# Kernel optimization log

Hardware: AMD Instinct MI355X
Metric: run time of the kernel (lower is better)

## Reference

```python
import jax, jax.numpy as jnp
import jax.lax as lax
import numpy as np
import math

B, T_FRAMES, H, W = 32, 8, 14, 14
C, CA = 768, 384
L = H * W + 1


def setup_inputs() -> dict:
    key = jax.random.key(0)
    ks = jax.random.split(key, 7)
    s = 0.02
    return {
        "x": jax.random.normal(ks[0], (B * T_FRAMES, L, C), dtype=jnp.float32),
        "W1": jax.random.normal(ks[1], (CA, C), dtype=jnp.float32) * s,
        "b1": jnp.zeros((CA,), dtype=jnp.float32),
        "conv_w": jax.random.normal(ks[2], (CA, 1, 3, 3, 3), dtype=jnp.float32) * s,
        "conv_b": jnp.zeros((CA,), dtype=jnp.float32),
        "W2": jax.random.normal(ks[3], (C, CA), dtype=jnp.float32) * s,
        "b2": jnp.zeros((C,), dtype=jnp.float32),
        "T": T_FRAMES,
    }


def reference(x, W1, b1, conv_w, conv_b, W2, b2, T):
    BT, Lx, Cx = x.shape
    Bb = BT // T
    Ca = W1.shape[0]
    Hh = Ww = int(round(math.sqrt(Lx - 1)))
    # fc1 on all tokens except CLS: [BT, L-1, Ca]
    h = jnp.einsum("blc,ac->bla", x[:, 1:, :], W1) + b1
    # -> [B, Ca, T, H, W] for depthwise 3d conv (groups = Ca)
    h = h.reshape(Bb, T, Hh, Ww, Ca).transpose(0, 4, 1, 2, 3)
    h = lax.conv_general_dilated(
        h, conv_w,
        window_strides=(1, 1, 1),
        padding=[(1, 1), (1, 1), (1, 1)],
        dimension_numbers=("NCDHW", "OIDHW", "NCDHW"),
        feature_group_count=Ca,
    ) + conv_b[None, :, None, None, None]
    # back to [BT, L-1, Ca]
    h = h.transpose(0, 2, 3, 4, 1).reshape(BT, Lx - 1, Ca)
    # fc2: [BT, L-1, C]
    h = jnp.einsum("bla,ca->blc", h, W2) + b2
    # residual add onto non-CLS tokens
    return x.at[:, 1:, :].add(h)
```

## Files before the change

### kernel.cpp

```cpp
#include <hip/hip_runtime.h>
#include <stdint.h>

#define BTOT   256
#define LX     197
#define CDIM   768
#define CADIM  384
#define TFR    8
#define HHH    14
#define WWW    14
#define LM1    196
#define MTOT   50176

typedef unsigned short u16;
typedef short          bf16x8 __attribute__((ext_vector_type(8)));
typedef unsigned short u16x4  __attribute__((ext_vector_type(4)));
typedef unsigned short u16x8  __attribute__((ext_vector_type(8)));
typedef float          f32x4  __attribute__((ext_vector_type(4)));

static __device__ __forceinline__ u16 f2bf(float f) {
  union { float f; uint32_t u; } v; v.f = f;
  uint32_t u = v.u;
  return (u16)((u + 0x7FFFu + ((u >> 16) & 1u)) >> 16);
}
static __device__ __forceinline__ float bf2f(u16 h) {
  union { uint32_t u; float f; } v; v.u = ((uint32_t)h) << 16;
  return v.f;
}

__global__ void prep_x(const float4* __restrict__ x, u16x4* __restrict__ xb, int nvec) {
  int stride = gridDim.x * blockDim.x;
  for (int i = blockIdx.x * blockDim.x + threadIdx.x; i < nvec; i += stride) {
    float4 v = x[i];
    u16x4 o;
    o[0] = f2bf(v.x); o[1] = f2bf(v.y); o[2] = f2bf(v.z); o[3] = f2bf(v.w);
    xb[i] = o;
  }
}

__global__ void prep_w(const float* __restrict__ W1, const float* __restrict__ W2,
                       const float* __restrict__ cw, u16* __restrict__ w1b,
                       u16* __restrict__ w2b, float* __restrict__ cwT) {
  int i = blockIdx.x * blockDim.x + threadIdx.x;
  if (i < CADIM * CDIM) { w1b[i] = f2bf(W1[i]); w2b[i] = f2bf(W2[i]); }
  if (i < CADIM * 27) {
    int a = i / 27; int tap = i - a * 27;
    cwT[tap * CADIM + a] = cw[i];
  }
}

__global__ void cls_copy(const float4* __restrict__ x, float4* __restrict__ out) {
  int i = blockIdx.x * blockDim.x + threadIdx.x;
  int bt = i / 192;
  int c  = i - bt * 192;
  int idx = bt * (LX * CDIM / 4) + c;
  out[idx] = x[idx];
}

#define BK  64
#define LDK 72

__global__ __launch_bounds__(256) void fc1_gemm(
    const u16* __restrict__ A,
    const u16* __restrict__ Bw,
    const float* __restrict__ bias,
    u16* __restrict__ Hout)
{
  __shared__ __align__(16) u16 As[128 * LDK];
  __shared__ __align__(16) u16 Bs[128 * LDK];
  const int tid = threadIdx.x;
  const int m0 = blockIdx.x * 128;
  const int n0 = blockIdx.y * 128;
  const int lane = tid & 63;
  const int wv = tid >> 6;
  const int wm = (wv & 1) * 64;
  const int wn = (wv >> 1) * 64;
  const int lm = lane & 15;
  const int lk = lane >> 4;

  f32x4 acc[4][4];
#pragma unroll
  for (int i = 0; i < 4; i++)
#pragma unroll
    for (int j = 0; j < 4; j++) acc[i][j] = (f32x4)0.0f;

  int arow_off[4], brow_off[4];
#pragma unroll
  for (int it = 0; it < 4; ++it) {
    int chunk = it * 256 + tid;
    int row = chunk >> 3;
    int tok = m0 + row;
    int bt = tok / LM1;
    int l = tok - bt * LM1;
    arow_off[it] = (bt * LX + 1 + l) * CDIM;
    brow_off[it] = (n0 + row) * CDIM;
  }

  for (int k0 = 0; k0 < CDIM; k0 += BK) {
#pragma unroll
    for (int it = 0; it < 4; ++it) {
      int chunk = it * 256 + tid;
      int row = chunk >> 3;
      int cc = chunk & 7;
      *(bf16x8*)&As[row * LDK + cc * 8] = *(const bf16x8*)(A + arow_off[it] + k0 + cc * 8);
      *(bf16x8*)&Bs[row * LDK + cc * 8] = *(const bf16x8*)(Bw + brow_off[it] + k0 + cc * 8);
    }
    __syncthreads();
#pragma unroll
    for (int kk = 0; kk < BK; kk += 32) {
      bf16x8 af[4], bfr[4];
#pragma unroll
      for (int i = 0; i < 4; i++)
        af[i] = *(const bf16x8*)&As[(wm + i * 16 + lm) * LDK + kk + lk * 8];
#pragma unroll
      for (int j = 0; j < 4; j++)
        bfr[j] = *(const bf16x8*)&Bs[(wn + j * 16 + lm) * LDK + kk + lk * 8];
#pragma unroll
      for (int i = 0; i < 4; i++)
#pragma unroll
        for (int j = 0; j < 4; j++)
          acc[i][j] = __builtin_amdgcn_mfma_f32_16x16x32_bf16(af[i], bfr[j], acc[i][j], 0, 0, 0);
    }
    __syncthreads();
  }

#pragma unroll
  for (int i = 0; i < 4; i++) {
    int rbase = m0 + wm + i * 16 + lk * 4;
#pragma unroll
    for (int j = 0; j < 4; j++) {
      int col = n0 + wn + j * 16 + lm;
      float bv = bias[col];
#pragma unroll
      for (int r = 0; r < 4; r++)
        Hout[(rbase + r) * CADIM + col] = f2bf(acc[i][j][r] + bv);
    }
  }
}

__global__ __launch_bounds__(256) void dwconv(
    const u16* __restrict__ h1, const float* __restrict__ cwT,
    const float* __restrict__ cb, u16* __restrict__ h2)
{
  int idx = blockIdx.x * blockDim.x + threadIdx.x;
  int tok = idx / 48;
  int cg = idx - tok * 48;
  int a0 = cg * 8;
  int bt = tok / LM1;
  int l = tok - bt * LM1;
  int t = bt & 7;
  int b = bt >> 3;
  int h = l / 14;
  int w = l - h * 14;

  float acc[8];
#pragma unroll
  for (int c = 0; c < 8; c++) acc[c] = cb[a0 + c];

#pragma unroll
  for (int dt = -1; dt <= 1; ++dt) {
    int tt = t + dt;
    if (tt < 0 || tt >= TFR) continue;
#pragma unroll
    for (int dh = -1; dh <= 1; ++dh) {
      int hh = h + dh;
      if (hh < 0 || hh >= HHH) continue;
#pragma unroll
      for (int dw = -1; dw <= 1; ++dw) {
        int ww = w + dw;
        if (ww < 0 || ww >= WWW) continue;
        int ntok = (b * TFR + tt) * LM1 + hh * 14 + ww;
        bf16x8 v = *(const bf16x8*)(h1 + ntok * CADIM + a0);
        int tap = (dt + 1) * 9 + (dh + 1) * 3 + (dw + 1);
        const float* wp = cwT + tap * CADIM + a0;
#pragma unroll
        for (int c = 0; c < 8; c++)
          acc[c] += bf2f((u16)v[c]) * wp[c];
      }
    }
  }
  u16x8 o;
#pragma unroll
  for (int c = 0; c < 8; c++) o[c] = f2bf(acc[c]);
  *(u16x8*)(h2 + tok * CADIM + a0) = o;
}

__global__ __launch_bounds__(256) void fc2_gemm(
    const u16* __restrict__ A,
    const u16* __restrict__ Bw,
    const float* __restrict__ bias,
    const float* __restrict__ x,
    float* __restrict__ out)
{
  __shared__ __align__(16) u16 As[128 * LDK];
  __shared__ __align__(16) u16 Bs[128 * LDK];
  const int tid = threadIdx.x;
  const int m0 = blockIdx.x * 128;
  const int n0 = blockIdx.y * 128;
  const int lane = tid & 63;
  const int wv = tid >> 6;
  const int wm = (wv & 1) * 64;
  const int wn = (wv >> 1) * 64;
  const int lm = lane & 15;
  const int lk = lane >> 4;

  f32x4 acc[4][4];
#pragma unroll
  for (int i = 0; i < 4; i++)
#pragma unroll
    for (int j = 0; j < 4; j++) acc[i][j] = (f32x4)0.0f;

  int arow_off[4], brow_off[4];
#pragma unroll
  for (int it = 0; it < 4; ++it) {
    int chunk = it * 256 + tid;
    int row = chunk >> 3;
    arow_off[it] = (m0 + row) * CADIM;
    brow_off[it] = (n0 + row) * CADIM;
  }

  for (int k0 = 0; k0 < CADIM; k0 += BK) {
#pragma unroll
    for (int it = 0; it < 4; ++it) {
      int chunk = it * 256 + tid;
      int row = chunk >> 3;
      int cc = chunk & 7;
      *(bf16x8*)&As[row * LDK + cc * 8] = *(const bf16x8*)(A + arow_off[it] + k0 + cc * 8);
      *(bf16x8*)&Bs[row * LDK + cc * 8] = *(const bf16x8*)(Bw + brow_off[it] + k0 + cc * 8);
    }
    __syncthreads();
#pragma unroll
    for (int kk = 0; kk < BK; kk += 32) {
      bf16x8 af[4], bfr[4];
#pragma unroll
      for (int i = 0; i < 4; i++)
        af[i] = *(const bf16x8*)&As[(wm + i * 16 + lm) * LDK + kk + lk * 8];
#pragma unroll
      for (int j = 0; j < 4; j++)
        bfr[j] = *(const bf16x8*)&Bs[(wn + j * 16 + lm) * LDK + kk + lk * 8];
#pragma unroll
      for (int i = 0; i < 4; i++)
#pragma unroll
        for (int j = 0; j < 4; j++)
          acc[i][j] = __builtin_amdgcn_mfma_f32_16x16x32_bf16(af[i], bfr[j], acc[i][j], 0, 0, 0);
    }
    __syncthreads();
  }

#pragma unroll
  for (int i = 0; i < 4; i++) {
    int rbase = m0 + wm + i * 16 + lk * 4;
#pragma unroll
    for (int r = 0; r < 4; r++) {
      int tok = rbase + r;
      int bt = tok / LM1;
      int l = tok - bt * LM1;
      int orow = (bt * LX + 1 + l) * CDIM;
#pragma unroll
      for (int j = 0; j < 4; j++) {
        int col = n0 + wn + j * 16 + lm;
        out[orow + col] = x[orow + col] + acc[i][j][r] + bias[col];
      }
    }
  }
}

extern "C" void kernel_launch(void* const* d_in, const int* in_sizes, int n_in,
                              void* d_out, int out_size, void* d_ws, size_t ws_size,
                              hipStream_t stream) {
  const float* x  = (const float*)d_in[0];
  const float* W1 = (const float*)d_in[1];
  const float* b1 = (const float*)d_in[2];
  const float* cw = (const float*)d_in[3];
  const float* cb = (const float*)d_in[4];
  const float* W2 = (const float*)d_in[5];
  const float* b2 = (const float*)d_in[6];
  float* out = (float*)d_out;

  char* ws = (char*)d_ws;
  u16*   xb  = (u16*)(ws + 0);
  u16*   w1b = (u16*)(ws + 77463552);
  u16*   w2b = (u16*)(ws + 78053376);
  float* cwT = (float*)(ws + 78643200);
  u16*   h1  = (u16*)(ws + 78684672);
  u16*   h2  = (u16*)(ws + 117219840);

  const int xelems = BTOT * LX * CDIM;

  prep_x  <<<2048, 256, 0, stream>>>((const float4*)x, (u16x4*)xb, xelems / 4);
  prep_w  <<<(CADIM * CDIM + 255) / 256, 256, 0, stream>>>(W1, W2, cw, w1b, w2b, cwT);
  cls_copy<<<(BTOT * 192) / 256, 256, 0, stream>>>((const float4*)x, (float4*)out);
  fc1_gemm<<<dim3(MTOT / 128, CADIM / 128), 256, 0, stream>>>(xb, w1b, b1, h1);
  dwconv  <<<(MTOT * 48) / 256, 256, 0, stream>>>(h1, cwT, cb, h2);
  fc2_gemm<<<dim3(MTOT / 128, CDIM / 128), 256, 0, stream>>>(h2, w2b, b2, x, out);
}
```

Before: 495.9 us.

## Use direct global-to-LDS loads with XOR swizzle, 2x2 register-tiled dwconv, fuse CLS copy

Result: faster. 473.7 us (-4.5%).

```diff
diff --git a/kernel.cpp b/kernel.cpp
--- a/kernel.cpp
+++ b/kernel.cpp
@@ -6,8 +6,6 @@
 #define CDIM   768
 #define CADIM  384
 #define TFR    8
-#define HHH    14
-#define WWW    14
 #define LM1    196
 #define MTOT   50176
 
@@ -17,6 +15,9 @@
 typedef unsigned short u16x8  __attribute__((ext_vector_type(8)));
 typedef float          f32x4  __attribute__((ext_vector_type(4)));
 
+typedef const __attribute__((address_space(1))) void gvoid_t;
+typedef __attribute__((address_space(3))) void       svoid_t;
+
 static __device__ __forceinline__ u16 f2bf(float f) {
   union { float f; uint32_t u; } v; v.f = f;
   uint32_t u = v.u;
@@ -27,13 +28,16 @@
   return v.f;
 }
 
-__global__ void prep_x(const float4* __restrict__ x, u16x4* __restrict__ xb, int nvec) {
+__global__ void prep_x(const float4* __restrict__ x, u16x4* __restrict__ xb,
+                       float4* __restrict__ out, int nvec) {
   int stride = gridDim.x * blockDim.x;
   for (int i = blockIdx.x * blockDim.x + threadIdx.x; i < nvec; i += stride) {
     float4 v = x[i];
     u16x4 o;
     o[0] = f2bf(v.x); o[1] = f2bf(v.y); o[2] = f2bf(v.z); o[3] = f2bf(v.w);
     xb[i] = o;
+    int rem = i % 37824;
+    if (rem < 192) out[i] = v;
   }
 }
 
@@ -48,16 +52,6 @@
   }
 }
 
-__global__ void cls_copy(const float4* __restrict__ x, float4* __restrict__ out) {
-  int i = blockIdx.x * blockDim.x + threadIdx.x;
-  int bt = i / 192;
-  int c  = i - bt * 192;
-  int idx = bt * (LX * CDIM / 4) + c;
-  out[idx] = x[idx];
-}
-
-#define BK  64
-#define LDK 72
 
 __global__ __launch_bounds__(256) void fc1_gemm(
     const u16* __restrict__ A,
@@ -65,55 +59,71 @@
     const float* __restrict__ bias,
     u16* __restrict__ Hout)
 {
-  __shared__ __align__(16) u16 As[128 * LDK];
-  __shared__ __align__(16) u16 Bs[128 * LDK];
-  const int tid = threadIdx.x;
+  __shared__ __align__(16) u16 As[128 * 64];
+  __shared__ __align__(16) u16 Bs[128 * 64];
+  const int tid  = threadIdx.x;
+  const int lane = tid & 63;
+  const int wave = tid >> 6;
   const int m0 = blockIdx.x * 128;
   const int n0 = blockIdx.y * 128;
-  const int lane = tid & 63;
-  const int wv = tid >> 6;
-  const int wm = (wv & 1) * 64;
-  const int wn = (wv >> 1) * 64;
   const int lm = lane & 15;
   const int lk = lane >> 4;
-
-  f32x4 acc[4][4];
-#pragma unroll
-  for (int i = 0; i < 4; i++)
-#pragma unroll
-    for (int j = 0; j < 4; j++) acc[i][j] = (f32x4)0.0f;
-
-  int arow_off[4], brow_off[4];
-#pragma unroll
-  for (int it = 0; it < 4; ++it) {
-    int chunk = it * 256 + tid;
-    int row = chunk >> 3;
+  const int wm = (wave & 1) * 64;
+  const int wn = (wave >> 1) * 64;
+
+  const int srow = lane >> 3;
+  const int cch  = (lane & 7) ^ srow;
+  size_t aoff[4], boff[4];
+  u16 *asdst[4], *bsdst[4];
+#pragma unroll
+  for (int s = 0; s < 4; ++s) {
+    int row = wave * 32 + s * 8 + srow;
     int tok = m0 + row;
     int bt = tok / LM1;
     int l = tok - bt * LM1;
-    arow_off[it] = (bt * LX + 1 + l) * CDIM;
-    brow_off[it] = (n0 + row) * CDIM;
-  }
-
-  for (int k0 = 0; k0 < CDIM; k0 += BK) {
-#pragma unroll
-    for (int it = 0; it < 4; ++it) {
-      int chunk = it * 256 + tid;
-      int row = chunk >> 3;
-      int cc = chunk & 7;
-      *(bf16x8*)&As[row * LDK + cc * 8] = *(const bf16x8*)(A + arow_off[it] + k0 + cc * 8);
-      *(bf16x8*)&Bs[row * LDK + cc * 8] = *(const bf16x8*)(Bw + brow_off[it] + k0 + cc * 8);
+    aoff[s] = (size_t)(bt * LX + 1 + l) * CDIM + cch * 8;
+    boff[s] = (size_t)(n0 + row) * CDIM + cch * 8;
+    asdst[s] = As + (wave * 32 + s * 8) * 64;
+    bsdst[s] = Bs + (wave * 32 + s * 8) * 64;
+  }
+  const int r7  = lm & 7;
+  const int sw0 = ((lk    ) ^ r7) << 3;
+  const int sw1 = ((lk + 4) ^ r7) << 3;
+
+  f32x4 acc[4][4];
+#pragma unroll
+  for (int i = 0; i < 4; i++)
+#pragma unroll
+    for (int j = 0; j < 4; j++) acc[i][j] = (f32x4)0.0f;
+
+  for (int k0 = 0; k0 < CDIM; k0 += 64) {
+#pragma unroll
+    for (int s = 0; s < 4; ++s) {
+      __builtin_amdgcn_global_load_lds((gvoid_t*)(A + aoff[s] + k0),
+                                       (svoid_t*)asdst[s], 16, 0, 0);
+      __builtin_amdgcn_global_load_lds((gvoid_t*)(Bw + boff[s] + k0),
+                                       (svoid_t*)bsdst[s], 16, 0, 0);
     }
     __syncthreads();
-#pragma unroll
-    for (int kk = 0; kk < BK; kk += 32) {
+    {
       bf16x8 af[4], bfr[4];
 #pragma unroll
       for (int i = 0; i < 4; i++)
-        af[i] = *(const bf16x8*)&As[(wm + i * 16 + lm) * LDK + kk + lk * 8];
+        af[i] = *(const bf16x8*)&As[(wm + i * 16 + lm) * 64 + sw0];
 #pragma unroll
       for (int j = 0; j < 4; j++)
-        bfr[j] = *(const bf16x8*)&Bs[(wn + j * 16 + lm) * LDK + kk + lk * 8];
+        bfr[j] = *(const bf16x8*)&Bs[(wn + j * 16 + lm) * 64 + sw0];
+#pragma unroll
+      for (int i = 0; i < 4; i++)
+#pragma unroll
+        for (int j = 0; j < 4; j++)
+          acc[i][j] = __builtin_amdgcn_mfma_f32_16x16x32_bf16(af[i], bfr[j], acc[i][j], 0, 0, 0);
+#pragma unroll
+      for (int i = 0; i < 4; i++)
+        af[i] = *(const bf16x8*)&As[(wm + i * 16 + lm) * 64 + sw1];
+#pragma unroll
+      for (int j = 0; j < 4; j++)
+        bfr[j] = *(const bf16x8*)&Bs[(wn + j * 16 + lm) * 64 + sw1];
 #pragma unroll
       for (int i = 0; i < 4; i++)
 #pragma unroll
@@ -142,46 +152,71 @@
     const float* __restrict__ cb, u16* __restrict__ h2)
 {
   int idx = blockIdx.x * blockDim.x + threadIdx.x;
-  int tok = idx / 48;
-  int cg = idx - tok * 48;
+  int cg = idx % 48;
+  int rest = idx / 48;
+  int wp = rest % 7; rest /= 7;
+  int hp = rest % 7; rest /= 7;
+  int t = rest & 7;
+  int frame = rest;
   int a0 = cg * 8;
-  int bt = tok / LM1;
-  int l = tok - bt * LM1;
-  int t = bt & 7;
-  int b = bt >> 3;
-  int h = l / 14;
-  int w = l - h * 14;
-
-  float acc[8];
-#pragma unroll
-  for (int c = 0; c < 8; c++) acc[c] = cb[a0 + c];
+  int h0 = hp * 2, w0 = wp * 2;
+
+  float acc[2][2][8];
+#pragma unroll
+  for (int c = 0; c < 8; ++c) {
+    float bv = cb[a0 + c];
+    acc[0][0][c] = bv; acc[0][1][c] = bv; acc[1][0][c] = bv; acc[1][1][c] = bv;
+  }
 
 #pragma unroll
   for (int dt = -1; dt <= 1; ++dt) {
     int tt = t + dt;
     if (tt < 0 || tt >= TFR) continue;
-#pragma unroll
-    for (int dh = -1; dh <= 1; ++dh) {
-      int hh = h + dh;
-      if (hh < 0 || hh >= HHH) continue;
-#pragma unroll
-      for (int dw = -1; dw <= 1; ++dw) {
-        int ww = w + dw;
-        if (ww < 0 || ww >= WWW) continue;
-        int ntok = (b * TFR + tt) * LM1 + hh * 14 + ww;
-        bf16x8 v = *(const bf16x8*)(h1 + ntok * CADIM + a0);
-        int tap = (dt + 1) * 9 + (dh + 1) * 3 + (dw + 1);
-        const float* wp = cwT + tap * CADIM + a0;
-#pragma unroll
-        for (int c = 0; c < 8; c++)
-          acc[c] += bf2f((u16)v[c]) * wp[c];
+    float wreg[9][8];
+#pragma unroll
+    for (int j = 0; j < 9; ++j) {
+      const float* wp8 = cwT + ((dt + 1) * 9 + j) * CADIM + a0;
+#pragma unroll
+      for (int c = 0; c < 8; ++c) wreg[j][c] = wp8[c];
+    }
+    const u16* fbase = h1 + (size_t)(frame + dt) * LM1 * CADIM + a0;
+#pragma unroll
+    for (int ih = 0; ih < 4; ++ih) {
+      int hh = h0 - 1 + ih;
+      if (hh < 0 || hh >= 14) continue;
+#pragma unroll
+      for (int iw = 0; iw < 4; ++iw) {
+        int ww = w0 - 1 + iw;
+        if (ww < 0 || ww >= 14) continue;
+        bf16x8 v = *(const bf16x8*)(fbase + (hh * 14 + ww) * CADIM);
+        float vf[8];
+#pragma unroll
+        for (int c = 0; c < 8; ++c) vf[c] = bf2f((u16)v[c]);
+#pragma unroll
+        for (int oh = 0; oh < 2; ++oh) {
+          if (ih - 1 - oh < -1 || ih - 1 - oh > 1) continue;
+#pragma unroll
+          for (int ow = 0; ow < 2; ++ow) {
+            if (iw - 1 - ow < -1 || iw - 1 - ow > 1) continue;
+            int j = (ih - oh) * 3 + (iw - ow);
+#pragma unroll
+            for (int c = 0; c < 8; ++c)
+              acc[oh][ow][c] += vf[c] * wreg[j][c];
+          }
+        }
       }
     }
   }
-  u16x8 o;
-#pragma unroll
-  for (int c = 0; c < 8; c++) o[c] = f2bf(acc[c]);
-  *(u16x8*)(h2 + tok * CADIM + a0) = o;
+  const size_t obase = (size_t)frame * LM1 * CADIM + a0;
+#pragma unroll
+  for (int oh = 0; oh < 2; ++oh)
+#pragma unroll
+    for (int ow = 0; ow < 2; ++ow) {
+      u16x8 o;
+#pragma unroll
+      for (int c = 0; c < 8; ++c) o[c] = f2bf(acc[oh][ow][c]);
+      *(u16x8*)(h2 + obase + ((size_t)(h0 + oh) * 14 + w0 + ow) * CADIM) = o;
+    }
 }
 
 __global__ __launch_bounds__(256) void fc2_gemm(
@@ -191,17 +226,33 @@
     const float* __restrict__ x,
     float* __restrict__ out)
 {
-  __shared__ __align__(16) u16 As[128 * LDK];
-  __shared__ __align__(16) u16 Bs[128 * LDK];
-  const int tid = threadIdx.x;
+  __shared__ __align__(16) u16 As[128 * 64];
+  __shared__ __align__(16) u16 Bs[128 * 64];
+  const int tid  = threadIdx.x;
+  const int lane = tid & 63;
+  const int wave = tid >> 6;
   const int m0 = blockIdx.x * 128;
   const int n0 = blockIdx.y * 128;
-  const int lane = tid & 63;
-  const int wv = tid >> 6;
-  const int wm = (wv & 1) * 64;
-  const int wn = (wv >> 1) * 64;
   const int lm = lane & 15;
   const int lk = lane >> 4;
+  const int wm = (wave & 1) * 64;
+  const int wn = (wave >> 1) * 64;
+
+  const int srow = lane >> 3;
+  const int cch  = (lane & 7) ^ srow;
+  size_t aoff[4], boff[4];
+  u16 *asdst[4], *bsdst[4];
+#pragma unroll
+  for (int s = 0; s < 4; ++s) {
+    int row = wave * 32 + s * 8 + srow;
+    aoff[s] = (size_t)(m0 + row) * CADIM + cch * 8;
+    boff[s] = (size_t)(n0 + row) * CADIM + cch * 8;
+    asdst[s] = As + (wave * 32 + s * 8) * 64;
+    bsdst[s] = Bs + (wave * 32 + s * 8) * 64;
+  }
+  const int r7  = lm & 7;
+  const int sw0 = ((lk    ) ^ r7) << 3;
+  const int sw1 = ((lk + 4) ^ r7) << 3;
 
   f32x4 acc[4][4];
 #pragma unroll
@@ -209,34 +260,34 @@
 #pragma unroll
     for (int j = 0; j < 4; j++) acc[i][j] = (f32x4)0.0f;
 
-  int arow_off[4], brow_off[4];
-#pragma unroll
-  for (int it = 0; it < 4; ++it) {
-    int chunk = it * 256 + tid;
-    int row = chunk >> 3;
-    arow_off[it] = (m0 + row) * CADIM;
-    brow_off[it] = (n0 + row) * CADIM;
-  }
-
-  for (int k0 = 0; k0 < CADIM; k0 += BK) {
-#pragma unroll
-    for (int it = 0; it < 4; ++it) {
-      int chunk = it * 256 + tid;
-      int row = chunk >> 3;
-      int cc = chunk & 7;
-      *(bf16x8*)&As[row * LDK + cc * 8] = *(const bf16x8*)(A + arow_off[it] + k0 + cc * 8);
-      *(bf16x8*)&Bs[row * LDK + cc * 8] = *(const bf16x8*)(Bw + brow_off[it] + k0 + cc * 8);
+  for (int k0 = 0; k0 < CADIM; k0 += 64) {
+#pragma unroll
+    for (int s = 0; s < 4; ++s) {
+      __builtin_amdgcn_global_load_lds((gvoid_t*)(A + aoff[s] + k0),
+                                       (svoid_t*)asdst[s], 16, 0, 0);
+      __builtin_amdgcn_global_load_lds((gvoid_t*)(Bw + boff[s] + k0),
+                                       (svoid_t*)bsdst[s], 16, 0, 0);
     }
     __syncthreads();
-#pragma unroll
-    for (int kk = 0; kk < BK; kk += 32) {
+    {
       bf16x8 af[4], bfr[4];
 #pragma unroll
       for (int i = 0; i < 4; i++)
-        af[i] = *(const bf16x8*)&As[(wm + i * 16 + lm) * LDK + kk + lk * 8];
+        af[i] = *(const bf16x8*)&As[(wm + i * 16 + lm) * 64 + sw0];
 #pragma unroll
       for (int j = 0; j < 4; j++)
-        bfr[j] = *(const bf16x8*)&Bs[(wn + j * 16 + lm) * LDK + kk + lk * 8];
+        bfr[j] = *(const bf16x8*)&Bs[(wn + j * 16 + lm) * 64 + sw0];
+#pragma unroll
+      for (int i = 0; i < 4; i++)
+#pragma unroll
+        for (int j = 0; j < 4; j++)
+          acc[i][j] = __builtin_amdgcn_mfma_f32_16x16x32_bf16(af[i], bfr[j], acc[i][j], 0, 0, 0);
+#pragma unroll
+      for (int i = 0; i < 4; i++)
+        af[i] = *(const bf16x8*)&As[(wm + i * 16 + lm) * 64 + sw1];
+#pragma unroll
+      for (int j = 0; j < 4; j++)
+        bfr[j] = *(const bf16x8*)&Bs[(wn + j * 16 + lm) * 64 + sw1];
 #pragma unroll
       for (int i = 0; i < 4; i++)
 #pragma unroll
@@ -254,7 +305,7 @@
       int tok = rbase + r;
       int bt = tok / LM1;
       int l = tok - bt * LM1;
-      int orow = (bt * LX + 1 + l) * CDIM;
+      size_t orow = (size_t)(bt * LX + 1 + l) * CDIM;
 #pragma unroll
       for (int j = 0; j < 4; j++) {
         int col = n0 + wn + j * 16 + lm;
@@ -286,10 +337,9 @@
 
   const int xelems = BTOT * LX * CDIM;
 
-  prep_x  <<<2048, 256, 0, stream>>>((const float4*)x, (u16x4*)xb, xelems / 4);
+  prep_x  <<<4096, 256, 0, stream>>>((const float4*)x, (u16x4*)xb, (float4*)out, xelems / 4);
   prep_w  <<<(CADIM * CDIM + 255) / 256, 256, 0, stream>>>(W1, W2, cw, w1b, w2b, cwT);
-  cls_copy<<<(BTOT * 192) / 256, 256, 0, stream>>>((const float4*)x, (float4*)out);
   fc1_gemm<<<dim3(MTOT / 128, CADIM / 128), 256, 0, stream>>>(xb, w1b, b1, h1);
-  dwconv  <<<(MTOT * 48) / 256, 256, 0, stream>>>(h1, cwT, cb, h2);
+  dwconv  <<<(BTOT * 49 * 48) / 256, 256, 0, stream>>>(h1, cwT, cb, h2);
   fc2_gemm<<<dim3(MTOT / 128, CDIM / 128), 256, 0, stream>>>(h2, w2b, b2, x, out);
 }
```
